# Performance work log

Hardware: AMD Instinct MI355X
Metric: run time of the kernel (lower is better)

Reference implementation:

```python
import jax, jax.numpy as jnp
import numpy as np

IN, HID, NCLS = 16, 50, 20


def setup_inputs() -> dict:
    key = jax.random.key(0)
    ks = jax.random.split(key, 7)
    B, T = 8192, 128
    s_ih = 1.0 / np.sqrt(HID)
    return {
        "x": jax.random.normal(ks[0], (B, T, IN), dtype=jnp.float32),
        # PyTorch LSTM params, gate order (i, f, g, o)
        "W_ih": jax.random.uniform(ks[1], (4 * HID, IN), jnp.float32, -s_ih, s_ih),
        "W_hh": jax.random.uniform(ks[2], (4 * HID, HID), jnp.float32, -s_ih, s_ih),
        "b_ih": jax.random.uniform(ks[3], (4 * HID,), jnp.float32, -s_ih, s_ih),
        "b_hh": jax.random.uniform(ks[4], (4 * HID,), jnp.float32, -s_ih, s_ih),
        "W_fc": jax.random.uniform(ks[5], (NCLS, HID), jnp.float32, -s_ih, s_ih),
        "b_fc": jax.random.uniform(ks[6], (NCLS,), jnp.float32, -s_ih, s_ih),
    }


def _lstm_last_hidden(x, W_ih, W_hh, b_ih, b_hh):
    # x: [B, T, IN] -> precompute input projections for all steps: [T, B, 4H]
    B = x.shape[0]
    xg = jnp.einsum("bti,gi->tbg", x, W_ih) + (b_ih + b_hh)

    def step(carry, xg_t):
        h, c = carry
        gates = xg_t + h @ W_hh.T  # [B, 4H]
        i, f, g, o = jnp.split(gates, 4, axis=-1)
        i = jax.nn.sigmoid(i)
        f = jax.nn.sigmoid(f)
        g = jnp.tanh(g)
        o = jax.nn.sigmoid(o)
        c = f * c + i * g
        h = o * jnp.tanh(c)
        return (h, c), None

    h0 = jnp.zeros((B, HID), x.dtype)
    c0 = jnp.zeros((B, HID), x.dtype)
    (hT, _), _ = jax.lax.scan(step, (h0, c0), xg)
    return hT  # == out[:, -1, :]


def reference(x, W_ih, W_hh, b_ih, b_hh, W_fc, b_fc):
    hT = _lstm_last_hidden(x.astype(jnp.float32), W_ih, W_hh, b_ih, b_hh)
    # dropout is identity in eval mode; relu then linear head on last timestep
    feat = jax.nn.relu(hT)
    logits = feat @ W_fc.T + b_fc  # [B, NCLS]
    return logits
```

## Files before the change

### kernel.cpp

```cpp
#include <hip/hip_runtime.h>

#define IN_    16
#define HID_   50
#define T_     128
#define NCLS_  20
#define BPB_   16
#define NTHR_  1024
#define NTILE_ 13
#define NQ_    2
#define KP_    72
#define KPW_   36

typedef _Float16 half8 __attribute__((ext_vector_type(8)));
typedef _Float16 h2_t  __attribute__((ext_vector_type(2)));
typedef float    f32x4 __attribute__((ext_vector_type(4)));
typedef unsigned int u32;

#define L2E_ 1.4426950408889634f
__device__ __forceinline__ h2_t as_h2(u32 v) { union { u32 u; h2_t h; } x; x.u = v; return x.h; }
__device__ __forceinline__ u32 pkh2(float a, float b) {
    union { u32 v; _Float16 h[2]; } p; p.h[0] = (_Float16)a; p.h[1] = (_Float16)b; return p.v;
}
#define FDOT2(S, W, ACC) __builtin_amdgcn_fdot2(as_h2(S), as_h2(W), (ACC), false)
#define MFMA(A, B, C) __builtin_amdgcn_mfma_f32_16x16x32_f16((A), (B), (C), 0, 0, 0)
#define SIGS(v)  __builtin_amdgcn_rcpf(1.0f + __builtin_amdgcn_exp2f(v))
#define TANHS(v) fmaf(2.0f, __builtin_amdgcn_rcpf(1.0f + __builtin_amdgcn_exp2f(v)), -1.0f)

__global__ __launch_bounds__(NTHR_, 8)
void lstm_mfma(const float* __restrict__ x,
               const float* __restrict__ W_ih,
               const float* __restrict__ W_hh,
               const float* __restrict__ b_ih,
               const float* __restrict__ b_hh,
               const float* __restrict__ W_fc,
               const float* __restrict__ b_fc,
               float* __restrict__ out)
{
    __shared__ __align__(16) _Float16 wfrag[NTILE_ * NQ_ * 64 * 8];
    __shared__ __align__(16) _Float16 st[2][BPB_ * KP_];

    const int tid  = threadIdx.x;
    const int lane = tid & 63;
    const int wv   = tid >> 6;
    const int b0   = blockIdx.x * BPB_;

    u32* wf32 = (u32*)wfrag;
    for (int idx = tid; idx < NTILE_ * NQ_ * 256; idx += NTHR_) {
        const int j    = idx & 3;
        const int ln   = (idx >> 2) & 63;
        const int chnk = idx >> 8;
        const int tile = chnk >> 1, q = chnk & 1;
        const int s  = tile * 16 + (ln & 15);
        const int u_ = s >> 2, kk = s & 3;
        const int k0 = q * 32 + (ln >> 4) * 8 + 2 * j;
        float w0 = 0.f, w1 = 0.f;
        if (u_ < HID_) {
            const int g = kk * HID_ + u_;
            w0 = (k0 < IN_) ? W_ih[g * IN_ + k0] : W_hh[g * HID_ + (k0 - IN_)];
            w1 = (k0 + 1 < IN_) ? W_ih[g * IN_ + k0 + 1] : W_hh[g * HID_ + (k0 + 1 - IN_)];
        }
        const float sc_ = (kk == 2) ? (-2.0f * L2E_) : (-L2E_);
        wf32[idx] = pkh2(w0 * sc_, w1 * sc_);
    }
    for (int idx = tid; idx < 2 * BPB_ * KPW_; idx += NTHR_)
        ((u32*)st)[idx] = 0u;

    const bool comp = (wv < NTILE_);
    const int  u    = 4 * wv + (lane >> 4);
    f32x4 bias = {0.f, 0.f, 0.f, 0.f};
    u32 wt0 = 0, wt1 = 0, wt2 = 0, wt3 = 0;
    if (comp && u < HID_) {
        bias[0] = (b_ih[u          ] + b_hh[u          ]) * -L2E_;
        bias[1] = (b_ih[HID_   + u ] + b_hh[HID_   + u ]) * -L2E_;
        bias[2] = (b_ih[2*HID_ + u ] + b_hh[2*HID_ + u ]) * (-2.0f * L2E_);
        bias[3] = (b_ih[3*HID_ + u ] + b_hh[3*HID_ + u ]) * -L2E_;
        wt0 = pkh2(W_hh[(u          ) * HID_ + 48] * -L2E_,          W_hh[(u          ) * HID_ + 49] * -L2E_);
        wt1 = pkh2(W_hh[(HID_   + u ) * HID_ + 48] * -L2E_,          W_hh[(HID_   + u ) * HID_ + 49] * -L2E_);
        wt2 = pkh2(W_hh[(2*HID_ + u ) * HID_ + 48] * (-2.0f * L2E_), W_hh[(2*HID_ + u ) * HID_ + 49] * (-2.0f * L2E_));
        wt3 = pkh2(W_hh[(3*HID_ + u ) * HID_ + 48] * -L2E_,          W_hh[(3*HID_ + u ) * HID_ + 49] * -L2E_);
    }
    float c_ = 0.f;

    const int bcol = lane & 15;
    const int brow = bcol * KP_ + (lane >> 4) * 8;
    const int trow = bcol * KPW_ + 32;
    const int hrow = bcol * KP_ + IN_ + u;
    const _Float16* wbase = wfrag + (size_t)(wv * NQ_) * 512 + lane * 8;

    const int  L  = tid - NTILE_ * 64;
    const bool xl = (!comp) && (L >= 0) && (L < BPB_ * 8);
    const int  bq = (L >> 3) & 15, fq = L & 7;
    const float* xq = x + (size_t)(b0 + bq) * (T_ * IN_) + 2 * fq;
    const int  xo = bq * KPW_ + fq;

    __syncthreads();

    half8 A0 = {}, A1 = {};
    if (comp) {
        A0 = *(const half8*)(wbase);
        A1 = *(const half8*)(wbase + 512);
    }
    if (xl) {
        const float2 v = *(const float2*)xq;
        ((u32*)st[0])[xo] = pkh2(v.x, v.y);
    }
    __syncthreads();

    for (int t = 0; t < T_; ++t) {
        const _Float16* sc = st[t & 1];
        _Float16*       sn = st[(t & 1) ^ 1];

        if (comp) {
            const half8 B0 = *(const half8*)(sc + brow);
            const half8 B1 = *(const half8*)(sc + brow + 32);
            const u32   hT = ((const u32*)sc)[trow];
            f32x4 C = MFMA(A0, B0, bias);
            C = MFMA(A1, B1, C);
            C[0] = FDOT2(hT, wt0, C[0]);
            C[1] = FDOT2(hT, wt1, C[1]);
            C[2] = FDOT2(hT, wt2, C[2]);
            C[3] = FDOT2(hT, wt3, C[3]);

            const float iv = SIGS(C[0]);
            const float fv = SIGS(C[1]);
            const float gv = TANHS(C[2]);
            const float ov = SIGS(C[3]);
            c_ = fmaf(fv, c_, iv * gv);
            const float hv = ov * TANHS(c_ * (-2.0f * L2E_));
            if (u < HID_) sn[hrow] = (_Float16)hv;
        } else if (xl && t + 1 < T_) {
            const float2 v = *(const float2*)(xq + (size_t)(t + 1) * IN_);
            ((u32*)sn)[xo] = pkh2(v.x, v.y);
        }
        __syncthreads();
    }

    const _Float16* hf = st[0];

    if (tid < BPB_ * NCLS_) {
        const int b  = tid / NCLS_;
        const int cl = tid - b * NCLS_;
        float acc = b_fc[cl];
        #pragma unroll
        for (int j = 0; j < HID_; ++j) {
            const float hv = fmaxf((float)hf[b * KP_ + IN_ + j], 0.0f);
            acc = fmaf(hv, W_fc[cl * HID_ + j], acc);
        }
        out[(size_t)(b0 + b) * NCLS_ + cl] = acc;
    }
}

extern "C" void kernel_launch(void* const* d_in, const int* in_sizes, int n_in,
                              void* d_out, int out_size, void* d_ws, size_t ws_size,
                              hipStream_t stream) {
    const float* x    = (const float*)d_in[0];
    const float* W_ih = (const float*)d_in[1];
    const float* W_hh = (const float*)d_in[2];
    const float* b_ih = (const float*)d_in[3];
    const float* b_hh = (const float*)d_in[4];
    const float* W_fc = (const float*)d_in[5];
    const float* b_fc = (const float*)d_in[6];
    float* out = (float*)d_out;

    const int B = in_sizes[0] / (T_ * IN_);
    dim3 grid(B / BPB_), block(NTHR_);
    hipLaunchKernelGGL(lstm_mfma, grid, block, 0, stream,
                       x, W_ih, W_hh, b_ih, b_hh, W_fc, b_fc, out);
}
```

Before: 103.2 us.

## Halve batch per block, give each wave two gate tiles, prefetch x into registers

Each block now handles 8 sequences with 512 threads instead of 16 with 1024. Seven compute waves each run two 16-row MFMA tiles (8 hidden units), and one wave loads x. The smaller per-step barrier and twice as many independent blocks aim to cut latency in the serial recurrence. The loader wave also prefetches the next timestep's x into registers one step ahead. The cost is that half of each MFMA's 16 batch columns are now redundant duplicates, so matrix work per useful sequence doubles.

```diff
diff --git a/kernel.cpp b/kernel.cpp
--- a/kernel.cpp
+++ b/kernel.cpp
@@ -4,9 +4,9 @@
 #define HID_   50
 #define T_     128
 #define NCLS_  20
-#define BPB_   16
-#define NTHR_  1024
-#define NTILE_ 13
+#define BPB_   8
+#define NTHR_  512
+#define NTILE_ 14
 #define NQ_    2
 #define KP_    72
 #define KPW_   36
@@ -65,44 +65,59 @@
     for (int idx = tid; idx < 2 * BPB_ * KPW_; idx += NTHR_)
         ((u32*)st)[idx] = 0u;
 
-    const bool comp = (wv < NTILE_);
-    const int  u    = 4 * wv + (lane >> 4);
-    f32x4 bias = {0.f, 0.f, 0.f, 0.f};
-    u32 wt0 = 0, wt1 = 0, wt2 = 0, wt3 = 0;
-    if (comp && u < HID_) {
-        bias[0] = (b_ih[u          ] + b_hh[u          ]) * -L2E_;
-        bias[1] = (b_ih[HID_   + u ] + b_hh[HID_   + u ]) * -L2E_;
-        bias[2] = (b_ih[2*HID_ + u ] + b_hh[2*HID_ + u ]) * (-2.0f * L2E_);
-        bias[3] = (b_ih[3*HID_ + u ] + b_hh[3*HID_ + u ]) * -L2E_;
-        wt0 = pkh2(W_hh[(u          ) * HID_ + 48] * -L2E_,          W_hh[(u          ) * HID_ + 49] * -L2E_);
-        wt1 = pkh2(W_hh[(HID_   + u ) * HID_ + 48] * -L2E_,          W_hh[(HID_   + u ) * HID_ + 49] * -L2E_);
-        wt2 = pkh2(W_hh[(2*HID_ + u ) * HID_ + 48] * (-2.0f * L2E_), W_hh[(2*HID_ + u ) * HID_ + 49] * (-2.0f * L2E_));
-        wt3 = pkh2(W_hh[(3*HID_ + u ) * HID_ + 48] * -L2E_,          W_hh[(3*HID_ + u ) * HID_ + 49] * -L2E_);
+    const bool comp = (wv < 7);
+    const int  u0   = 8 * wv + (lane >> 4);
+    const int  u1   = u0 + 4;
+    f32x4 bias0 = {0.f,0.f,0.f,0.f}, bias1 = {0.f,0.f,0.f,0.f};
+    u32 ta0=0,ta1=0,ta2=0,ta3=0, tb0=0,tb1=0,tb2=0,tb3=0;
+    if (comp && u0 < HID_) {
+        bias0[0] = (b_ih[u0         ] + b_hh[u0         ]) * -L2E_;
+        bias0[1] = (b_ih[HID_  + u0 ] + b_hh[HID_  + u0 ]) * -L2E_;
+        bias0[2] = (b_ih[2*HID_+ u0 ] + b_hh[2*HID_+ u0 ]) * (-2.0f * L2E_);
+        bias0[3] = (b_ih[3*HID_+ u0 ] + b_hh[3*HID_+ u0 ]) * -L2E_;
+        ta0 = pkh2(W_hh[(u0         ) * HID_ + 48] * -L2E_,          W_hh[(u0         ) * HID_ + 49] * -L2E_);
+        ta1 = pkh2(W_hh[(HID_  + u0 ) * HID_ + 48] * -L2E_,          W_hh[(HID_  + u0 ) * HID_ + 49] * -L2E_);
+        ta2 = pkh2(W_hh[(2*HID_+ u0 ) * HID_ + 48] * (-2.0f * L2E_), W_hh[(2*HID_+ u0 ) * HID_ + 49] * (-2.0f * L2E_));
+        ta3 = pkh2(W_hh[(3*HID_+ u0 ) * HID_ + 48] * -L2E_,          W_hh[(3*HID_+ u0 ) * HID_ + 49] * -L2E_);
     }
-    float c_ = 0.f;
+    if (comp && u1 < HID_) {
+        bias1[0] = (b_ih[u1         ] + b_hh[u1         ]) * -L2E_;
+        bias1[1] = (b_ih[HID_  + u1 ] + b_hh[HID_  + u1 ]) * -L2E_;
+        bias1[2] = (b_ih[2*HID_+ u1 ] + b_hh[2*HID_+ u1 ]) * (-2.0f * L2E_);
+        bias1[3] = (b_ih[3*HID_+ u1 ] + b_hh[3*HID_+ u1 ]) * -L2E_;
+        tb0 = pkh2(W_hh[(u1         ) * HID_ + 48] * -L2E_,          W_hh[(u1         ) * HID_ + 49] * -L2E_);
+        tb1 = pkh2(W_hh[(HID_  + u1 ) * HID_ + 48] * -L2E_,          W_hh[(HID_  + u1 ) * HID_ + 49] * -L2E_);
+        tb2 = pkh2(W_hh[(2*HID_+ u1 ) * HID_ + 48] * (-2.0f * L2E_), W_hh[(2*HID_+ u1 ) * HID_ + 49] * (-2.0f * L2E_));
+        tb3 = pkh2(W_hh[(3*HID_+ u1 ) * HID_ + 48] * -L2E_,          W_hh[(3*HID_+ u1 ) * HID_ + 49] * -L2E_);
+    }
+    float c0_ = 0.f, c1_ = 0.f;
 
-    const int bcol = lane & 15;
-    const int brow = bcol * KP_ + (lane >> 4) * 8;
-    const int trow = bcol * KPW_ + 32;
-    const int hrow = bcol * KP_ + IN_ + u;
-    const _Float16* wbase = wfrag + (size_t)(wv * NQ_) * 512 + lane * 8;
+    const int  bcol = lane & 7;
+    const int  brow = bcol * KP_ + (lane >> 4) * 8;
+    const int  trow = bcol * KPW_ + 32;
+    const bool wrt  = ((lane & 8) == 0);
+    const int  hrow0 = bcol * KP_ + IN_ + u0;
+    const int  hrow1 = bcol * KP_ + IN_ + u1;
+    const _Float16* wbase = wfrag + (size_t)(4 * wv) * 512 + lane * 8;
 
-    const int  L  = tid - NTILE_ * 64;
-    const bool xl = (!comp) && (L >= 0) && (L < BPB_ * 8);
-    const int  bq = (L >> 3) & 15, fq = L & 7;
+    const int bq = lane >> 3, fq = lane & 7;
     const float* xq = x + (size_t)(b0 + bq) * (T_ * IN_) + 2 * fq;
-    const int  xo = bq * KPW_ + fq;
+    const int xo = bq * KPW_ + fq;
 
     __syncthreads();
 
-    half8 A0 = {}, A1 = {};
+    half8 A0 = {}, A1 = {}, A2 = {}, A3 = {};
     if (comp) {
         A0 = *(const half8*)(wbase);
         A1 = *(const half8*)(wbase + 512);
+        A2 = *(const half8*)(wbase + 1024);
+        A3 = *(const half8*)(wbase + 1536);
     }
-    if (xl) {
+    float2 xr = make_float2(0.f, 0.f);
+    if (!comp) {
         const float2 v = *(const float2*)xq;
         ((u32*)st[0])[xo] = pkh2(v.x, v.y);
+        xr = *(const float2*)(xq + IN_);
     }
     __syncthreads();
 
@@ -114,23 +129,36 @@
             const half8 B0 = *(const half8*)(sc + brow);
             const half8 B1 = *(const half8*)(sc + brow + 32);
             const u32   hT = ((const u32*)sc)[trow];
-            f32x4 C = MFMA(A0, B0, bias);
-            C = MFMA(A1, B1, C);
-            C[0] = FDOT2(hT, wt0, C[0]);
-            C[1] = FDOT2(hT, wt1, C[1]);
-            C[2] = FDOT2(hT, wt2, C[2]);
-            C[3] = FDOT2(hT, wt3, C[3]);
+            f32x4 C0 = MFMA(A0, B0, bias0);
+            C0 = MFMA(A1, B1, C0);
+            f32x4 C1 = MFMA(A2, B0, bias1);
+            C1 = MFMA(A3, B1, C1);
+            C0[0] = FDOT2(hT, ta0, C0[0]);
+            C0[1] = FDOT2(hT, ta1, C0[1]);
+            C0[2] = FDOT2(hT, ta2, C0[2]);
+            C0[3] = FDOT2(hT, ta3, C0[3]);
+            C1[0] = FDOT2(hT, tb0, C1[0]);
+            C1[1] = FDOT2(hT, tb1, C1[1]);
+            C1[2] = FDOT2(hT, tb2, C1[2]);
+            C1[3] = FDOT2(hT, tb3, C1[3]);
 
-            const float iv = SIGS(C[0]);
-            const float fv = SIGS(C[1]);
-            const float gv = TANHS(C[2]);
-            const float ov = SIGS(C[3]);
-            c_ = fmaf(fv, c_, iv * gv);
-            const float hv = ov * TANHS(c_ * (-2.0f * L2E_));
-            if (u < HID_) sn[hrow] = (_Float16)hv;
-        } else if (xl && t + 1 < T_) {
-            const float2 v = *(const float2*)(xq + (size_t)(t + 1) * IN_);
-            ((u32*)sn)[xo] = pkh2(v.x, v.y);
+            {
+                const float iv = SIGS(C0[0]), fv = SIGS(C0[1]);
+                const float gv = TANHS(C0[2]), ov = SIGS(C0[3]);
+                c0_ = fmaf(fv, c0_, iv * gv);
+                const float hv = ov * TANHS(c0_ * (-2.0f * L2E_));
+                if (wrt && u0 < HID_) sn[hrow0] = (_Float16)hv;
+            }
+            {
+                const float iv = SIGS(C1[0]), fv = SIGS(C1[1]);
+                const float gv = TANHS(C1[2]), ov = SIGS(C1[3]);
+                c1_ = fmaf(fv, c1_, iv * gv);
+                const float hv = ov * TANHS(c1_ * (-2.0f * L2E_));
+                if (wrt && u1 < HID_) sn[hrow1] = (_Float16)hv;
+            }
+        } else {
+            if (t + 1 < T_) ((u32*)sn)[xo] = pkh2(xr.x, xr.y);
+            if (t + 2 < T_) xr = *(const float2*)(xq + (size_t)(t + 2) * IN_);
         }
         __syncthreads();
     }
```

Result: slower. 179.1 us (+73.5%).

## Process two batch groups per block sharing weights, prefetch x in registers

Applied to the files above, without the earlier changes.

Each block now handles two 16-sample groups, so every compute wave issues two independent MFMA chains per timestep that reuse the same weight fragments, and the per-step barrier cost is spread over twice the batch. Weight fragments are loaded straight from global into registers, which removes the LDS staging array. The x-loader wave keeps the next step's input in registers and loads one step further ahead to hide global latency. The block shrinks to 14 waves with occupancy bound 4, and the grid halves, which lowers parallelism across the device.

```diff
diff --git a/kernel.cpp b/kernel.cpp
--- a/kernel.cpp
+++ b/kernel.cpp
@@ -4,10 +4,10 @@
 #define HID_   50
 #define T_     128
 #define NCLS_  20
-#define BPB_   16
-#define NTHR_  1024
-#define NTILE_ 13
-#define NQ_    2
+#define GRP_   16
+#define NGRP_  2
+#define BPB_   (GRP_ * NGRP_)
+#define NTHR_  896
 #define KP_    72
 #define KPW_   36
 
@@ -26,7 +26,7 @@
 #define SIGS(v)  __builtin_amdgcn_rcpf(1.0f + __builtin_amdgcn_exp2f(v))
 #define TANHS(v) fmaf(2.0f, __builtin_amdgcn_rcpf(1.0f + __builtin_amdgcn_exp2f(v)), -1.0f)
 
-__global__ __launch_bounds__(NTHR_, 8)
+__global__ __launch_bounds__(NTHR_, 4)
 void lstm_mfma(const float* __restrict__ x,
                const float* __restrict__ W_ih,
                const float* __restrict__ W_hh,
@@ -36,37 +36,39 @@
                const float* __restrict__ b_fc,
                float* __restrict__ out)
 {
-    __shared__ __align__(16) _Float16 wfrag[NTILE_ * NQ_ * 64 * 8];
-    __shared__ __align__(16) _Float16 st[2][BPB_ * KP_];
+    __shared__ __align__(16) _Float16 st[NGRP_][2][GRP_ * KP_];
 
     const int tid  = threadIdx.x;
     const int lane = tid & 63;
     const int wv   = tid >> 6;
     const int b0   = blockIdx.x * BPB_;
+    const bool comp = (wv < 13);
 
-    u32* wf32 = (u32*)wfrag;
-    for (int idx = tid; idx < NTILE_ * NQ_ * 256; idx += NTHR_) {
-        const int j    = idx & 3;
-        const int ln   = (idx >> 2) & 63;
-        const int chnk = idx >> 8;
-        const int tile = chnk >> 1, q = chnk & 1;
-        const int s  = tile * 16 + (ln & 15);
-        const int u_ = s >> 2, kk = s & 3;
-        const int k0 = q * 32 + (ln >> 4) * 8 + 2 * j;
-        float w0 = 0.f, w1 = 0.f;
-        if (u_ < HID_) {
-            const int g = kk * HID_ + u_;
-            w0 = (k0 < IN_) ? W_ih[g * IN_ + k0] : W_hh[g * HID_ + (k0 - IN_)];
-            w1 = (k0 + 1 < IN_) ? W_ih[g * IN_ + k0 + 1] : W_hh[g * HID_ + (k0 + 1 - IN_)];
-        }
-        const float sc_ = (kk == 2) ? (-2.0f * L2E_) : (-L2E_);
-        wf32[idx] = pkh2(w0 * sc_, w1 * sc_);
-    }
-    for (int idx = tid; idx < 2 * BPB_ * KPW_; idx += NTHR_)
+    for (int idx = tid; idx < NGRP_ * 2 * GRP_ * KPW_; idx += NTHR_)
         ((u32*)st)[idx] = 0u;
 
-    const bool comp = (wv < NTILE_);
-    const int  u    = 4 * wv + (lane >> 4);
+    half8 A0 = {}, A1 = {};
+    if (comp) {
+        const int sA = wv * 16 + (lane & 15);
+        const int uA = sA >> 2, kA = sA & 3;
+        if (uA < HID_) {
+            const float scA = (kA == 2) ? (-2.0f * L2E_) : (-L2E_);
+            const int g  = kA * HID_ + uA;
+            const int k0 = (lane >> 4) * 8;
+            const float* s0 = (k0 < IN_) ? (W_ih + g * IN_ + k0)
+                                         : (W_hh + g * HID_ + (k0 - IN_));
+            const float* s1 = W_hh + g * HID_ + 16 + (lane >> 4) * 8;
+            #pragma unroll
+            for (int e = 0; e < 4; ++e) {
+                const float2 p0 = *(const float2*)(s0 + 2 * e);
+                const float2 p1 = *(const float2*)(s1 + 2 * e);
+                A0[2*e] = (_Float16)(p0.x * scA); A0[2*e+1] = (_Float16)(p0.y * scA);
+                A1[2*e] = (_Float16)(p1.x * scA); A1[2*e+1] = (_Float16)(p1.y * scA);
+            }
+        }
+    }
+
+    const int u = comp ? (4 * wv + (lane >> 4)) : 0;
     f32x4 bias = {0.f, 0.f, 0.f, 0.f};
     u32 wt0 = 0, wt1 = 0, wt2 = 0, wt3 = 0;
     if (comp && u < HID_) {
@@ -79,71 +81,90 @@
         wt2 = pkh2(W_hh[(2*HID_ + u ) * HID_ + 48] * (-2.0f * L2E_), W_hh[(2*HID_ + u ) * HID_ + 49] * (-2.0f * L2E_));
         wt3 = pkh2(W_hh[(3*HID_ + u ) * HID_ + 48] * -L2E_,          W_hh[(3*HID_ + u ) * HID_ + 49] * -L2E_);
     }
-    float c_ = 0.f;
+    float cA = 0.f, cB = 0.f;
 
     const int bcol = lane & 15;
     const int brow = bcol * KP_ + (lane >> 4) * 8;
     const int trow = bcol * KPW_ + 32;
     const int hrow = bcol * KP_ + IN_ + u;
-    const _Float16* wbase = wfrag + (size_t)(wv * NQ_) * 512 + lane * 8;
 
-    const int  L  = tid - NTILE_ * 64;
-    const bool xl = (!comp) && (L >= 0) && (L < BPB_ * 8);
-    const int  bq = (L >> 3) & 15, fq = L & 7;
-    const float* xq = x + (size_t)(b0 + bq) * (T_ * IN_) + 2 * fq;
-    const int  xo = bq * KPW_ + fq;
+    const int  lb  = lane >> 1;
+    const int  lg  = lb >> 4;
+    const int  lbc = lb & 15;
+    const int  lfh = (lane & 1) * 8;
+    const float* xq = x + (size_t)(b0 + lb) * (T_ * IN_) + lfh;
+    const int  xo  = lbc * KPW_ + (lfh >> 1);
 
+    float4 xr0 = {0,0,0,0}, xr1 = {0,0,0,0};
     __syncthreads();
-
-    half8 A0 = {}, A1 = {};
-    if (comp) {
-        A0 = *(const half8*)(wbase);
-        A1 = *(const half8*)(wbase + 512);
-    }
-    if (xl) {
-        const float2 v = *(const float2*)xq;
-        ((u32*)st[0])[xo] = pkh2(v.x, v.y);
+    if (!comp) {
+        const float4 v0 = *(const float4*)(xq);
+        const float4 v1 = *(const float4*)(xq + 4);
+        u32* d = (u32*)st[lg][0];
+        d[xo] = pkh2(v0.x, v0.y); d[xo+1] = pkh2(v0.z, v0.w);
+        d[xo+2] = pkh2(v1.x, v1.y); d[xo+3] = pkh2(v1.z, v1.w);
+        xr0 = *(const float4*)(xq + IN_);
+        xr1 = *(const float4*)(xq + IN_ + 4);
     }
     __syncthreads();
 
     for (int t = 0; t < T_; ++t) {
-        const _Float16* sc = st[t & 1];
-        _Float16*       sn = st[(t & 1) ^ 1];
+        const int cur = t & 1, nxt = cur ^ 1;
 
         if (comp) {
-            const half8 B0 = *(const half8*)(sc + brow);
-            const half8 B1 = *(const half8*)(sc + brow + 32);
-            const u32   hT = ((const u32*)sc)[trow];
-            f32x4 C = MFMA(A0, B0, bias);
-            C = MFMA(A1, B1, C);
-            C[0] = FDOT2(hT, wt0, C[0]);
-            C[1] = FDOT2(hT, wt1, C[1]);
-            C[2] = FDOT2(hT, wt2, C[2]);
-            C[3] = FDOT2(hT, wt3, C[3]);
+            const _Float16* scA_ = st[0][cur];
+            const half8 Ba0 = *(const half8*)(scA_ + brow);
+            const half8 Ba1 = *(const half8*)(scA_ + brow + 32);
+            const u32   hTa = ((const u32*)scA_)[trow];
+            const _Float16* scB_ = st[1][cur];
+            const half8 Bb0 = *(const half8*)(scB_ + brow);
+            const half8 Bb1 = *(const half8*)(scB_ + brow + 32);
+            const u32   hTb = ((const u32*)scB_)[trow];
 
-            const float iv = SIGS(C[0]);
-            const float fv = SIGS(C[1]);
-            const float gv = TANHS(C[2]);
-            const float ov = SIGS(C[3]);
-            c_ = fmaf(fv, c_, iv * gv);
-            const float hv = ov * TANHS(c_ * (-2.0f * L2E_));
-            if (u < HID_) sn[hrow] = (_Float16)hv;
-        } else if (xl && t + 1 < T_) {
-            const float2 v = *(const float2*)(xq + (size_t)(t + 1) * IN_);
-            ((u32*)sn)[xo] = pkh2(v.x, v.y);
+            f32x4 Ca = MFMA(A0, Ba0, bias);
+            f32x4 Cb = MFMA(A0, Bb0, bias);
+            Ca = MFMA(A1, Ba1, Ca);
+            Cb = MFMA(A1, Bb1, Cb);
+            Ca[0] = FDOT2(hTa, wt0, Ca[0]);  Cb[0] = FDOT2(hTb, wt0, Cb[0]);
+            Ca[1] = FDOT2(hTa, wt1, Ca[1]);  Cb[1] = FDOT2(hTb, wt1, Cb[1]);
+            Ca[2] = FDOT2(hTa, wt2, Ca[2]);  Cb[2] = FDOT2(hTb, wt2, Cb[2]);
+            Ca[3] = FDOT2(hTa, wt3, Ca[3]);  Cb[3] = FDOT2(hTb, wt3, Cb[3]);
+
+            const float ia = SIGS(Ca[0]), fa = SIGS(Ca[1]);
+            const float ib = SIGS(Cb[0]), fb = SIGS(Cb[1]);
+            const float ga = TANHS(Ca[2]), oa = SIGS(Ca[3]);
+            const float gb = TANHS(Cb[2]), ob = SIGS(Cb[3]);
+            cA = fmaf(fa, cA, ia * ga);
+            cB = fmaf(fb, cB, ib * gb);
+            const float ha = oa * TANHS(cA * (-2.0f * L2E_));
+            const float hb = ob * TANHS(cB * (-2.0f * L2E_));
+            if (u < HID_) {
+                st[0][nxt][hrow] = (_Float16)ha;
+                st[1][nxt][hrow] = (_Float16)hb;
+            }
+        } else {
+            if (t + 1 < T_) {
+                u32* d = (u32*)st[lg][nxt];
+                d[xo] = pkh2(xr0.x, xr0.y); d[xo+1] = pkh2(xr0.z, xr0.w);
+                d[xo+2] = pkh2(xr1.x, xr1.y); d[xo+3] = pkh2(xr1.z, xr1.w);
+            }
+            if (t + 2 < T_) {
+                xr0 = *(const float4*)(xq + (size_t)(t + 2) * IN_);
+                xr1 = *(const float4*)(xq + (size_t)(t + 2) * IN_ + 4);
+            }
         }
         __syncthreads();
     }
 
-    const _Float16* hf = st[0];
-
     if (tid < BPB_ * NCLS_) {
         const int b  = tid / NCLS_;
         const int cl = tid - b * NCLS_;
+        const _Float16* hf = st[b >> 4][0];
+        const int bc = b & 15;
         float acc = b_fc[cl];
         #pragma unroll
         for (int j = 0; j < HID_; ++j) {
-            const float hv = fmaxf((float)hf[b * KP_ + IN_ + j], 0.0f);
+            const float hv = fmaxf((float)hf[bc * KP_ + IN_ + j], 0.0f);
             acc = fmaf(hv, W_fc[cl * HID_ + j], acc);
         }
         out[(size_t)(b0 + b) * NCLS_ + cl] = acc;
```

Measured after the change: 107.9 us. 4.6% more time.
